# Optimization experiments

Hardware: AMD Instinct MI355X
Metric: run time of the kernel (lower is better)

The kernel has to match this reference:

```python
import jax, jax.numpy as jnp
import numpy as np

N = 4096
IN_DIM = 256
OUT_DIM = 256
E = 131072


def setup_inputs() -> dict:
    key = jax.random.key(0)
    ks = jax.random.split(key, 8)
    x = jax.random.normal(ks[0], (N, IN_DIM), dtype=jnp.float32)
    edge_index = jax.random.randint(ks[1], (2, E), 0, N, dtype=jnp.int64)
    lap = jax.random.normal(ks[2], (N, N), dtype=jnp.float32)
    d_inv = jax.random.normal(ks[3], (N, N), dtype=jnp.float32)
    # parameters
    W_high = jax.random.normal(ks[4], (IN_DIM, OUT_DIM), dtype=jnp.float32) / np.sqrt(IN_DIM)
    W_conv = jax.random.normal(ks[5], (IN_DIM, OUT_DIM), dtype=jnp.float32) / np.sqrt(IN_DIM)
    b_conv = jnp.zeros((OUT_DIM,), dtype=jnp.float32)
    aL = jax.random.uniform(ks[6], (1,), dtype=jnp.float32)
    aH = jax.random.uniform(ks[7], (1,), dtype=jnp.float32)
    return {"x": x, "edge_index": edge_index, "lap": lap, "d_inv": d_inv,
            "W_high": W_high, "W_conv": W_conv, "b_conv": b_conv,
            "aL": aL, "aH": aH}


def _gcn_conv(x, edge_index, W, b, num_nodes):
    # PyG GCNConv: add self-loops, symmetric normalization, aggregate at target.
    src, dst = edge_index[0], edge_index[1]
    loop = jnp.arange(num_nodes, dtype=edge_index.dtype)
    src_f = jnp.concatenate([src, loop])
    dst_f = jnp.concatenate([dst, loop])
    deg = jax.ops.segment_sum(jnp.ones_like(dst_f, dtype=x.dtype), dst_f,
                              num_segments=num_nodes)
    deg_inv_sqrt = jnp.where(deg > 0, jax.lax.rsqrt(jnp.maximum(deg, 1e-12)), 0.0)
    norm = deg_inv_sqrt[src_f] * deg_inv_sqrt[dst_f]  # [E+N]
    xw = x @ W                                        # [N, out]
    msgs = xw[src_f] * norm[:, None]                  # [E+N, out]
    out = jax.ops.segment_sum(msgs, dst_f, num_segments=num_nodes)
    return out + b


def reference(x, edge_index, lap, d_inv, W_high, W_conv, b_conv, aL, aH):
    # high-pass branch: Lhp = d_inv @ lap @ d_inv; Hh = Lhp @ relu(x @ W_high)
    Lhp = (d_inv @ lap) @ d_inv
    Hh = Lhp @ jax.nn.relu(x @ W_high)
    # low-pass branch: GCNConv
    Hl = _gcn_conv(x, edge_index, W_conv, b_conv, x.shape[0])
    return aL * Hl + aH * Hh
```

## Files before the change

kernel.cpp:

```cpp
#include <hip/hip_runtime.h>

#define NN 4096
#define DD 256
#define EE 131072

typedef __attribute__((ext_vector_type(8))) short s16x8;
typedef __attribute__((ext_vector_type(4))) float f32x4;

__device__ __forceinline__ unsigned short f2bf(float f) {
  unsigned u = __builtin_bit_cast(unsigned, f);
  u += 0x7FFFu + ((u >> 16) & 1u);
  return (unsigned short)(u >> 16);
}

__device__ __forceinline__ ushort4 cvt4(f32x4 v) {
  ushort4 r;
  r.x = f2bf(v[0]); r.y = f2bf(v[1]); r.z = f2bf(v[2]); r.w = f2bf(v[3]);
  return r;
}

__device__ __forceinline__ unsigned cvt2_rhu(float a, float b) {
  unsigned ua = __builtin_bit_cast(unsigned, a) + 0x8000u;
  unsigned ub = __builtin_bit_cast(unsigned, b) + 0x8000u;
  return __builtin_amdgcn_perm(ub, ua, 0x07060302u);
}

__device__ __forceinline__ uint4 pack8(f32x4 a, f32x4 b) {
  uint4 r;
  r.x = cvt2_rhu(a[0], a[1]); r.y = cvt2_rhu(a[2], a[3]);
  r.z = cvt2_rhu(b[0], b[1]); r.w = cvt2_rhu(b[2], b[3]);
  return r;
}


__global__ void k_prep(const int* __restrict__ ei, int* __restrict__ deg,
                       const float* __restrict__ Wh, const float* __restrict__ Wc,
                       unsigned short* __restrict__ WFh, unsigned short* __restrict__ WFc) {
  int t = blockIdx.x * 256 + threadIdx.x;
  if (t < EE) {
    atomicAdd(&deg[ei[EE + t]], 1);
  } else {
    int idx = t - EE;
    int which = idx >> 16;
    int r = idx & 65535;
    int n = r & 255, k = r >> 8;
    const float* W = which ? Wc : Wh;
    unsigned short* WF = which ? WFc : WFh;
    long fidx = ((long)((n >> 4) * 8 + (k >> 5))) * 512 +
                (((k >> 3) & 3) * 16 + (n & 15)) * 8 + (k & 7);
    WF[fidx] = f2bf(W[k * 256 + n]);
  }
}

__global__ void k_scan(const int* __restrict__ deg, int* __restrict__ row_start,
                       float* __restrict__ dis) {
  __shared__ int part[1024];
  int t = threadIdx.x;
  int d0 = deg[4 * t + 0], d1 = deg[4 * t + 1], d2 = deg[4 * t + 2], d3 = deg[4 * t + 3];
  int s = d0 + d1 + d2 + d3;
  part[t] = s;
  __syncthreads();
  for (int off = 1; off < 1024; off <<= 1) {
    int add = (t >= off) ? part[t - off] : 0;
    __syncthreads();
    part[t] += add;
    __syncthreads();
  }
  int base = part[t] - s;
  row_start[4 * t + 0] = base;
  row_start[4 * t + 1] = base + d0;
  row_start[4 * t + 2] = base + d0 + d1;
  row_start[4 * t + 3] = base + d0 + d1 + d2;
  if (t == 1023) row_start[4096] = part[t];
  dis[4 * t + 0] = rsqrtf((float)d0 + 1.0f);
  dis[4 * t + 1] = rsqrtf((float)d1 + 1.0f);
  dis[4 * t + 2] = rsqrtf((float)d2 + 1.0f);
  dis[4 * t + 3] = rsqrtf((float)d3 + 1.0f);
}

__global__ void k_scatter(const int* __restrict__ ei, const int* __restrict__ row_start,
                          int* __restrict__ cursor, int* __restrict__ csr) {
  int e = blockIdx.x * 256 + threadIdx.x;
  if (e < EE) {
    int s = ei[e];
    int d = ei[EE + e];
    int p = atomicAdd(&cursor[d], 1);
    csr[row_start[d] + p] = s;
  }
}

__global__ __launch_bounds__(512) void k_xw(const float* __restrict__ x,
                                            const unsigned short* __restrict__ WFh,
                                            const unsigned short* __restrict__ WFc,
                                            unsigned short* __restrict__ RF,
                                            float* __restrict__ XWs,
                                            const float* __restrict__ dis) {
  __shared__ alignas(16) unsigned short Abuf[16][264];
  const int tid = threadIdx.x;
  const int w = tid >> 6, lane = tid & 63;
  const int quad = lane >> 4, l16 = lane & 15, quad8 = quad * 8;
  const int m0 = blockIdx.x * 16;

  {
    int srow = tid >> 5, scolf = (tid & 31) * 8;
    const float* ap = x + (long)(m0 + srow) * DD + scolf;
    f32x4 a0 = *(const f32x4*)ap;
    f32x4 a1 = *(const f32x4*)(ap + 4);
    *(uint4*)&Abuf[srow][scolf] = pack8(a0, a1);
  }
  __syncthreads();

  const bool hi = (w < 4);
  const int wo = hi ? w : (w - 4);
  const unsigned short* WF = hi ? WFh : WFc;
  const unsigned short* bp = WF + lane * 8;

  f32x4 acc[4] = {{0,0,0,0},{0,0,0,0},{0,0,0,0},{0,0,0,0}};
#pragma unroll
  for (int q = 0; q < 8; ++q) {
    s16x8 af = *(const s16x8*)&Abuf[l16][q * 32 + quad8];
#pragma unroll
    for (int s = 0; s < 4; ++s) {
      s16x8 bf = *(const s16x8*)(bp + ((long)((4 * wo + s) * 8 + q)) * 512);
      acc[s] = __builtin_amdgcn_mfma_f32_16x16x32_bf16(af, bf, acc[s], 0, 0, 0);
    }
  }

  if (hi) {
    const int kc = m0 >> 5;
    const int qp = ((m0 >> 4) & 1) * 2 + (quad >> 1);
    const int j0 = (quad & 1) * 4;
#pragma unroll
    for (int s = 0; s < 4; ++s) {
      int t = 4 * wo + s;
      f32x4 v = acc[s];
      f32x4 z;
      z[0] = v[0] > 0.f ? v[0] : 0.f;
      z[1] = v[1] > 0.f ? v[1] : 0.f;
      z[2] = v[2] > 0.f ? v[2] : 0.f;
      z[3] = v[3] > 0.f ? v[3] : 0.f;
      long idx = ((long)(t * 128 + kc)) * 512 + (qp * 16 + l16) * 8 + j0;
      *(ushort4*)(RF + idx) = cvt4(z);
    }
  } else {
    float dm[4];
#pragma unroll
    for (int r = 0; r < 4; ++r) dm[r] = dis[m0 + quad * 4 + r];
#pragma unroll
    for (int s = 0; s < 4; ++s) {
      int col = 64 * wo + 16 * s + l16;
#pragma unroll
      for (int r = 0; r < 4; ++r)
        XWs[(long)(m0 + quad * 4 + r) * DD + col] = dm[r] * acc[s][r];
    }
  }
}

__global__ void k_agg(const float* __restrict__ XWs, const int* __restrict__ row_start,
                      const int* __restrict__ csr, const float* __restrict__ dis,
                      float* __restrict__ Hl) {
  const int i = blockIdx.x;
  const int t = threadIdx.x;
  const int b0 = row_start[i], b1 = row_start[i + 1];
  float acc = XWs[(long)i * DD + t];
  int j = b0;
  for (; j + 4 <= b1; j += 4) {
    int s0 = csr[j], s1 = csr[j + 1], s2 = csr[j + 2], s3 = csr[j + 3];
    float v0 = XWs[(long)s0 * DD + t];
    float v1 = XWs[(long)s1 * DD + t];
    float v2 = XWs[(long)s2 * DD + t];
    float v3 = XWs[(long)s3 * DD + t];
    acc += (v0 + v1) + (v2 + v3);
  }
  for (; j < b1; ++j) acc += XWs[(long)csr[j] * DD + t];
  Hl[(long)i * DD + t] = dis[i] * acc;
}

template <int EPI>
__global__ __launch_bounds__(512) void k_mm2(const float* __restrict__ A,
                                             const unsigned short* __restrict__ BF,
                                             unsigned short* __restrict__ CF,
                                             float* __restrict__ outF,
                                             const float* __restrict__ Hl,
                                             const float* __restrict__ bconv,
                                             const float* __restrict__ aLp,
                                             const float* __restrict__ aHp) {
  __shared__ alignas(16) unsigned short Abuf[2][32][264];
  const int tid = threadIdx.x;
  const int w = tid >> 6, lane = tid & 63;
  const int quad = lane >> 4, l16 = lane & 15, quad8 = quad * 8;
  const int tile = blockIdx.x & 127, half = blockIdx.x >> 7;
  const int m0 = tile * 32;
  const int tglob = half * 8 + w;

  const int arow = tid >> 4;
  const int acolf = (tid & 15) * 16;
  const float* aptr = A + (long)(m0 + arow) * NN + acolf;

  {
    f32x4 c0 = *(const f32x4*)(aptr + 0);
    f32x4 c1 = *(const f32x4*)(aptr + 4);
    f32x4 c2 = *(const f32x4*)(aptr + 8);
    f32x4 c3 = *(const f32x4*)(aptr + 12);
    *(uint4*)&Abuf[0][arow][acolf] = pack8(c0, c1);
    *(uint4*)&Abuf[0][arow][acolf + 8] = pack8(c2, c3);
  }
  f32x4 anext[4];
#pragma unroll
  for (int i = 0; i < 4; ++i) anext[i] = *(const f32x4*)(aptr + 256 + 4 * i);
  __syncthreads();

  f32x4 acc[2] = {{0,0,0,0},{0,0,0,0}};
  const unsigned short* bbase = BF + ((long)tglob * 128) * 512 + lane * 8;

  for (int s = 0; s < 16; ++s) {
    const int cur = s & 1;
    f32x4 afut[4];
    if (s + 2 < 16) {
#pragma unroll
      for (int i = 0; i < 4; ++i)
        afut[i] = *(const f32x4*)(aptr + (s + 2) * 256 + 4 * i);
    } else {
#pragma unroll
      for (int i = 0; i < 4; ++i) afut[i] = anext[i];
    }

    const unsigned short* bs = bbase + ((long)s * 8) * 512;
#pragma unroll
    for (int c8 = 0; c8 < 8; ++c8) {
      s16x8 bf = *(const s16x8*)(bs + c8 * 512);
      s16x8 a0 = *(const s16x8*)&Abuf[cur][l16][c8 * 32 + quad8];
      s16x8 a1 = *(const s16x8*)&Abuf[cur][16 + l16][c8 * 32 + quad8];
      acc[0] = __builtin_amdgcn_mfma_f32_16x16x32_bf16(a0, bf, acc[0], 0, 0, 0);
      acc[1] = __builtin_amdgcn_mfma_f32_16x16x32_bf16(a1, bf, acc[1], 0, 0, 0);
    }

    if (s + 1 < 16) {
      *(uint4*)&Abuf[1 - cur][arow][acolf] = pack8(anext[0], anext[1]);
      *(uint4*)&Abuf[1 - cur][arow][acolf + 8] = pack8(anext[2], anext[3]);
    }
    __syncthreads();
#pragma unroll
    for (int i = 0; i < 4; ++i) anext[i] = afut[i];
  }

  if constexpr (EPI == 0) {
    const int kc = m0 >> 5;
#pragma unroll
    for (int mu = 0; mu < 2; ++mu) {
      int qp = mu * 2 + (quad >> 1);
      int j0 = (quad & 1) * 4;
      long idx = ((long)(tglob * 128 + kc)) * 512 + (qp * 16 + l16) * 8 + j0;
      *(ushort4*)(CF + idx) = cvt4(acc[mu]);
    }
  } else {
    __shared__ float obuf[32][132];
#pragma unroll
    for (int mu = 0; mu < 2; ++mu)
#pragma unroll
      for (int r = 0; r < 4; ++r)
        obuf[mu * 16 + quad * 4 + r][w * 16 + l16] = acc[mu][r];
    __syncthreads();
    const float aLv = aLp[0], aHv = aHp[0];
    const int orow = tid >> 4;
    const int ocol = (tid & 15) * 8;
    const int gcol = half * 128 + ocol;
#pragma unroll
    for (int j = 0; j < 2; ++j) {
      f32x4 cc = *(const f32x4*)&obuf[orow][ocol + 4 * j];
      f32x4 h = *(const f32x4*)(Hl + (long)(m0 + orow) * DD + gcol + 4 * j);
      f32x4 bc = *(const f32x4*)(bconv + gcol + 4 * j);
      f32x4 res;
      res[0] = aHv * cc[0] + aLv * (h[0] + bc[0]);
      res[1] = aHv * cc[1] + aLv * (h[1] + bc[1]);
      res[2] = aHv * cc[2] + aLv * (h[2] + bc[2]);
      res[3] = aHv * cc[3] + aLv * (h[3] + bc[3]);
      *(f32x4*)(outF + (long)(m0 + orow) * DD + gcol + 4 * j) = res;
    }
  }
}

extern "C" void kernel_launch(void* const* d_in, const int* in_sizes, int n_in,
                              void* d_out, int out_size, void* d_ws, size_t ws_size,
                              hipStream_t stream) {
  const float* x     = (const float*)d_in[0];
  const int*   ei    = (const int*)d_in[1];
  const float* lap   = (const float*)d_in[2];
  const float* dinv  = (const float*)d_in[3];
  const float* Wh    = (const float*)d_in[4];
  const float* Wc    = (const float*)d_in[5];
  const float* bconv = (const float*)d_in[6];
  const float* aL    = (const float*)d_in[7];
  const float* aH    = (const float*)d_in[8];
  float* out = (float*)d_out;
  char* ws = (char*)d_ws;

  int* deg        = (int*)(ws);
  int* cursor     = (int*)(ws + (16 << 10));
  int* row_start  = (int*)(ws + (32 << 10));
  int* csr        = (int*)(ws + (64 << 10));
  float* dis      = (float*)(ws + (576 << 10));
  unsigned short* WFh = (unsigned short*)(ws + (1l << 20));
  unsigned short* WFc = (unsigned short*)(ws + (1l << 20) + (128 << 10));
  unsigned short* RF  = (unsigned short*)(ws + (2l << 20));
  unsigned short* T1F = (unsigned short*)(ws + (4l << 20));
  unsigned short* T2F = (unsigned short*)(ws + (6l << 20));
  float* XWs = (float*)(ws + (8l << 20));
  float* Hl  = (float*)(ws + (12l << 20));

  hipMemsetAsync(ws, 0, 32 << 10, stream);

  k_prep<<<1024, 256, 0, stream>>>(ei, deg, Wh, Wc, WFh, WFc);
  k_scan<<<1, 1024, 0, stream>>>(deg, row_start, dis);
  k_scatter<<<512, 256, 0, stream>>>(ei, row_start, cursor, csr);
  k_xw<<<256, 512, 0, stream>>>(x, WFh, WFc, RF, XWs, dis);
  k_agg<<<4096, 256, 0, stream>>>(XWs, row_start, csr, dis, Hl);

  k_mm2<0><<<256, 512, 0, stream>>>(dinv, RF, T1F, nullptr, nullptr, nullptr, nullptr, nullptr);
  k_mm2<0><<<256, 512, 0, stream>>>(lap, T1F, T2F, nullptr, nullptr, nullptr, nullptr, nullptr);
  k_mm2<3><<<256, 512, 0, stream>>>(dinv, T2F, nullptr, out, Hl, bconv, aL, aH);
}
```

Measured before the change: 274.9 us.

## Halve GEMM row tile to 16 and double grid for more blocks per CU

The row tile of the dense bf16 MFMA GEMM kernel shrinks from 32 to 16 rows, and each launch grows from 256 to 512 blocks. Each wave now issues one MFMA per K-chunk instead of two, and the A staging buffer is halved. The epilogue buffer reuses the A shared memory. The aim is more resident blocks per CU to hide global-load latency on the fp32 A stream, at the cost of reading the B panel twice as often and less MFMA work per A load.

Result: slower. 280.6 us (+2.1%).

```diff
diff --git a/kernel.cpp b/kernel.cpp
--- a/kernel.cpp
+++ b/kernel.cpp
@@ -185,98 +185,83 @@
                                              const float* __restrict__ bconv,
                                              const float* __restrict__ aLp,
                                              const float* __restrict__ aHp) {
-  __shared__ alignas(16) unsigned short Abuf[2][32][264];
+  __shared__ alignas(16) unsigned short Abuf[2][16][264];
   const int tid = threadIdx.x;
   const int w = tid >> 6, lane = tid & 63;
   const int quad = lane >> 4, l16 = lane & 15, quad8 = quad * 8;
-  const int tile = blockIdx.x & 127, half = blockIdx.x >> 7;
-  const int m0 = tile * 32;
+  const int tile = blockIdx.x & 255, half = blockIdx.x >> 8;
+  const int m0 = tile * 16;
   const int tglob = half * 8 + w;
 
-  const int arow = tid >> 4;
-  const int acolf = (tid & 15) * 16;
+  const int arow = tid >> 5;
+  const int acolf = (tid & 31) * 8;
   const float* aptr = A + (long)(m0 + arow) * NN + acolf;
 
   {
     f32x4 c0 = *(const f32x4*)(aptr + 0);
     f32x4 c1 = *(const f32x4*)(aptr + 4);
-    f32x4 c2 = *(const f32x4*)(aptr + 8);
-    f32x4 c3 = *(const f32x4*)(aptr + 12);
     *(uint4*)&Abuf[0][arow][acolf] = pack8(c0, c1);
-    *(uint4*)&Abuf[0][arow][acolf + 8] = pack8(c2, c3);
-  }
-  f32x4 anext[4];
-#pragma unroll
-  for (int i = 0; i < 4; ++i) anext[i] = *(const f32x4*)(aptr + 256 + 4 * i);
+  }
+  f32x4 anext[2];
+  anext[0] = *(const f32x4*)(aptr + 256);
+  anext[1] = *(const f32x4*)(aptr + 260);
   __syncthreads();
 
-  f32x4 acc[2] = {{0,0,0,0},{0,0,0,0}};
+  f32x4 acc = {0, 0, 0, 0};
   const unsigned short* bbase = BF + ((long)tglob * 128) * 512 + lane * 8;
 
   for (int s = 0; s < 16; ++s) {
     const int cur = s & 1;
-    f32x4 afut[4];
+    f32x4 afut[2];
     if (s + 2 < 16) {
-#pragma unroll
-      for (int i = 0; i < 4; ++i)
-        afut[i] = *(const f32x4*)(aptr + (s + 2) * 256 + 4 * i);
+      afut[0] = *(const f32x4*)(aptr + (s + 2) * 256);
+      afut[1] = *(const f32x4*)(aptr + (s + 2) * 256 + 4);
     } else {
-#pragma unroll
-      for (int i = 0; i < 4; ++i) afut[i] = anext[i];
+      afut[0] = anext[0];
+      afut[1] = anext[1];
     }
 
     const unsigned short* bs = bbase + ((long)s * 8) * 512;
 #pragma unroll
-    for (int c8 = 0; c8 < 8; ++c8) {
-      s16x8 bf = *(const s16x8*)(bs + c8 * 512);
-      s16x8 a0 = *(const s16x8*)&Abuf[cur][l16][c8 * 32 + quad8];
-      s16x8 a1 = *(const s16x8*)&Abuf[cur][16 + l16][c8 * 32 + quad8];
-      acc[0] = __builtin_amdgcn_mfma_f32_16x16x32_bf16(a0, bf, acc[0], 0, 0, 0);
-      acc[1] = __builtin_amdgcn_mfma_f32_16x16x32_bf16(a1, bf, acc[1], 0, 0, 0);
+    for (int q = 0; q < 8; ++q) {
+      s16x8 bf = *(const s16x8*)(bs + q * 512);
+      s16x8 af = *(const s16x8*)&Abuf[cur][l16][q * 32 + quad8];
+      acc = __builtin_amdgcn_mfma_f32_16x16x32_bf16(af, bf, acc, 0, 0, 0);
     }
 
     if (s + 1 < 16) {
       *(uint4*)&Abuf[1 - cur][arow][acolf] = pack8(anext[0], anext[1]);
-      *(uint4*)&Abuf[1 - cur][arow][acolf + 8] = pack8(anext[2], anext[3]);
     }
     __syncthreads();
-#pragma unroll
-    for (int i = 0; i < 4; ++i) anext[i] = afut[i];
+    anext[0] = afut[0];
+    anext[1] = afut[1];
   }
 
   if constexpr (EPI == 0) {
-    const int kc = m0 >> 5;
-#pragma unroll
-    for (int mu = 0; mu < 2; ++mu) {
-      int qp = mu * 2 + (quad >> 1);
-      int j0 = (quad & 1) * 4;
-      long idx = ((long)(tglob * 128 + kc)) * 512 + (qp * 16 + l16) * 8 + j0;
-      *(ushort4*)(CF + idx) = cvt4(acc[mu]);
-    }
+    const int kc = tile >> 1;
+    const int qp = (tile & 1) * 2 + (quad >> 1);
+    const int j0 = (quad & 1) * 4;
+    long idx = ((long)(tglob * 128 + kc)) * 512 + (qp * 16 + l16) * 8 + j0;
+    *(ushort4*)(CF + idx) = cvt4(acc);
   } else {
-    __shared__ float obuf[32][132];
-#pragma unroll
-    for (int mu = 0; mu < 2; ++mu)
-#pragma unroll
-      for (int r = 0; r < 4; ++r)
-        obuf[mu * 16 + quad * 4 + r][w * 16 + l16] = acc[mu][r];
+    float(*obuf)[132] = reinterpret_cast<float(*)[132]>(&Abuf[0][0][0]);
+#pragma unroll
+    for (int r = 0; r < 4; ++r)
+      obuf[quad * 4 + r][w * 16 + l16] = acc[r];
     __syncthreads();
     const float aLv = aLp[0], aHv = aHp[0];
-    const int orow = tid >> 4;
-    const int ocol = (tid & 15) * 8;
+    const int orow = tid >> 5;
+    const int ocol = (tid & 31) * 4;
     const int gcol = half * 128 + ocol;
-#pragma unroll
-    for (int j = 0; j < 2; ++j) {
-      f32x4 cc = *(const f32x4*)&obuf[orow][ocol + 4 * j];
-      f32x4 h = *(const f32x4*)(Hl + (long)(m0 + orow) * DD + gcol + 4 * j);
-      f32x4 bc = *(const f32x4*)(bconv + gcol + 4 * j);
-      f32x4 res;
-      res[0] = aHv * cc[0] + aLv * (h[0] + bc[0]);
-      res[1] = aHv * cc[1] + aLv * (h[1] + bc[1]);
-      res[2] = aHv * cc[2] + aLv * (h[2] + bc[2]);
-      res[3] = aHv * cc[3] + aLv * (h[3] + bc[3]);
-      *(f32x4*)(outF + (long)(m0 + orow) * DD + gcol + 4 * j) = res;
-    }
+    f32x4 cc = *(const f32x4*)&obuf[orow][ocol];
+    f32x4 h = *(const f32x4*)(Hl + (long)(m0 + orow) * DD + gcol);
+    f32x4 bc = *(const f32x4*)(bconv + gcol);
+    f32x4 res;
+    res[0] = aHv * cc[0] + aLv * (h[0] + bc[0]);
+    res[1] = aHv * cc[1] + aLv * (h[1] + bc[1]);
+    res[2] = aHv * cc[2] + aLv * (h[2] + bc[2]);
+    res[3] = aHv * cc[3] + aLv * (h[3] + bc[3]);
+    *(f32x4*)(outF + (long)(m0 + orow) * DD + gcol) = res;
   }
 }
 
@@ -316,7 +301,7 @@
   k_xw<<<256, 512, 0, stream>>>(x, WFh, WFc, RF, XWs, dis);
   k_agg<<<4096, 256, 0, stream>>>(XWs, row_start, csr, dis, Hl);
 
-  k_mm2<0><<<256, 512, 0, stream>>>(dinv, RF, T1F, nullptr, nullptr, nullptr, nullptr, nullptr);
-  k_mm2<0><<<256, 512, 0, stream>>>(lap, T1F, T2F, nullptr, nullptr, nullptr, nullptr, nullptr);
-  k_mm2<3><<<256, 512, 0, stream>>>(dinv, T2F, nullptr, out, Hl, bconv, aL, aH);
-}
+  k_mm2<0><<<512, 512, 0, stream>>>(dinv, RF, T1F, nullptr, nullptr, nullptr, nullptr, nullptr);
+  k_mm2<0><<<512, 512, 0, stream>>>(lap, T1F, T2F, nullptr, nullptr, nullptr, nullptr, nullptr);
+  k_mm2<3><<<512, 512, 0, stream>>>(dinv, T2F, nullptr, out, Hl, bconv, aL, aH);
+}
```
